# Kernel tuning notes

Measured on AMD Instinct MI355X. Metric: run time of the kernel, lower is better.

Reference implementation:

```python
import jax, jax.numpy as jnp
import numpy as np

NEG_SLOPE = 0.2  # PyG GATv2Conv default negative_slope


def _gatv2(h, src, dst, Wl, bl, Wr, br, att, bias, N):
    """GATv2Conv (concat=True). h: [N,Fin]; att: [H,F]; returns [N,H*F]."""
    H, F = att.shape
    xl = (h @ Wl + bl).reshape(N, H, F)  # source transform
    xr = (h @ Wr + br).reshape(N, H, F)  # target transform
    # per-edge GATv2 score: a^T LeakyReLU(xl[src] + xr[dst])
    e = jax.nn.leaky_relu(xl[src] + xr[dst], negative_slope=NEG_SLOPE)  # [E,H,F]
    logits = jnp.einsum('ehf,hf->eh', e, att)  # [E,H]
    # segment softmax over destination nodes (self-loops guarantee nonempty segments)
    m = jax.ops.segment_max(logits, dst, num_segments=N)  # [N,H]
    p = jnp.exp(logits - m[dst])
    s = jax.ops.segment_sum(p, dst, num_segments=N)  # [N,H]
    alpha = p / s[dst]  # [E,H]
    out = jax.ops.segment_sum(alpha[:, :, None] * xl[src], dst, num_segments=N)  # [N,H,F]
    return out.reshape(N, H * F) + bias


def setup_inputs() -> dict:
    key = jax.random.key(0)
    ks = jax.random.split(key, 16)
    N, E = 30000, 480000
    L, D, H, F = 50, 100, 3, 100
    W = D * H  # 300
    sc = 0.1  # keep activations stable through 5 layers
    return {
        'x': jax.random.randint(ks[0], (N,), 0, L),
        'edge_index': jax.random.randint(ks[1], (2, E), 0, N),
        'emb': jax.random.normal(ks[2], (L, D), jnp.float32),
        'Wl0': jax.random.normal(ks[3], (D, W), jnp.float32) * sc,
        'bl0': jnp.zeros((W,), jnp.float32),
        'Wr0': jax.random.normal(ks[4], (D, W), jnp.float32) * sc,
        'br0': jnp.zeros((W,), jnp.float32),
        'att0': jax.random.normal(ks[5], (H, F), jnp.float32) * sc,
        'bias0': jnp.zeros((W,), jnp.float32),
        'Wl': jax.random.normal(ks[6], (4, W, W), jnp.float32) * sc,
        'bl': jnp.zeros((4, W), jnp.float32),
        'Wr': jax.random.normal(ks[7], (4, W, W), jnp.float32) * sc,
        'br': jnp.zeros((4, W), jnp.float32),
        'att': jax.random.normal(ks[8], (4, H, F), jnp.float32) * sc,
        'bias': jnp.zeros((4, W), jnp.float32),
    }


def reference(x, edge_index, emb, Wl0, bl0, Wr0, br0, att0, bias0,
              Wl, bl, Wr, br, att, bias):
    N = x.shape[0]
    loops = jnp.arange(N)
    src = jnp.concatenate([edge_index[0], loops])  # PyG add_self_loops=True
    dst = jnp.concatenate([edge_index[1], loops])
    h = emb[x]  # node_embedding(x).squeeze()
    h = jax.nn.relu(_gatv2(h, src, dst, Wl0, bl0, Wr0, br0, att0, bias0, N))
    for i in range(4):  # remaining num_gnn_layers-1 convs, each followed by ReLU
        h = jax.nn.relu(_gatv2(h, src, dst, Wl[i], bl[i], Wr[i], br[i], att[i], bias[i], N))
    return h  # [N, heads*hidden] = [N, 300]
```

## Files before the change

kernel.cpp:

```cpp
#include <hip/hip_runtime.h>

#define NODES   30000
#define E0N     480000
#define ETOT    510000
#define D0      100
#define WDIM    300
#define NW      600
#define NEG     0.2f

typedef __bf16 bf16x8 __attribute__((ext_vector_type(8)));
typedef float  f32x4  __attribute__((ext_vector_type(4)));

__global__ void count_edges(const int* __restrict__ ei, int* __restrict__ counts) {
    int e = blockIdx.x * 256 + threadIdx.x;
    if (e >= ETOT) return;
    int d = (e < E0N) ? ei[E0N + e] : (e - E0N);
    atomicAdd(&counts[d], 1);
}

__global__ __launch_bounds__(1024) void scan_kernel(const int* __restrict__ counts,
                                                    int* __restrict__ offsets, int n) {
    __shared__ int lds[1024];
    const int CH = 32;
    int t = threadIdx.x;
    int base = t * CH;
    int loc[CH];
    int sum = 0;
    #pragma unroll
    for (int i = 0; i < CH; i++) {
        int v = (base + i < n) ? counts[base + i] : 0;
        loc[i] = sum;
        sum += v;
    }
    lds[t] = sum;
    __syncthreads();
    for (int off = 1; off < 1024; off <<= 1) {
        int v = (t >= off) ? lds[t - off] : 0;
        __syncthreads();
        lds[t] += v;
        __syncthreads();
    }
    int ex = (t == 0) ? 0 : lds[t - 1];
    #pragma unroll
    for (int i = 0; i < CH; i++) {
        int idx = base + i;
        if (idx < n) offsets[idx] = ex + loc[i];
    }
    if (t == 0) offsets[n] = lds[1023];
}

__global__ void scatter_edges(const int* __restrict__ ei, const int* __restrict__ offsets,
                              int* __restrict__ cursor, int* __restrict__ csr_src) {
    int e = blockIdx.x * 256 + threadIdx.x;
    if (e >= ETOT) return;
    int s, d;
    if (e < E0N) { s = ei[e]; d = ei[E0N + e]; }
    else         { s = e - E0N; d = s; }
    int pos = offsets[d] + atomicAdd(&cursor[d], 1);
    csr_src[pos] = s;
}

__global__ void make_bfrag(const float* __restrict__ Bl, const float* __restrict__ Br,
                           bf16x8* __restrict__ out, int K, int ksteps) {
    int t = blockIdx.x * 256 + threadIdx.x;
    int total = ksteps * 40 * 64;
    if (t >= total) return;
    int lane = t & 63;
    int n16  = (t >> 6) % 40;
    int s    = t / (64 * 40);
    int c = n16 * 16 + (lane & 15);
    union { bf16x8 v; __bf16 e[8]; } hi, lo;
    #pragma unroll
    for (int j = 0; j < 8; j++) {
        int k = s * 32 + ((lane >> 4) * 8) + j;
        float x = 0.f;
        if (k < K && c < NW)
            x = (c < WDIM) ? Bl[(size_t)k * WDIM + c] : Br[(size_t)k * WDIM + c - WDIM];
        __bf16 h = (__bf16)x;
        hi.e[j] = h;
        lo.e[j] = (__bf16)(x - (float)h);
    }
    size_t base = ((size_t)(s * 40 + n16) * 2) * 64 + lane;
    out[base]      = hi.v;
    out[base + 64] = lo.v;
}

__global__ __launch_bounds__(256) void gemm_mfma(
    const float* __restrict__ A, const int* __restrict__ xmap, int use_map,
    const bf16x8* __restrict__ Bfrag,
    const float* __restrict__ bl, const float* __restrict__ br,
    float* __restrict__ Cl, float* __restrict__ Cr,
    int M, int K, int ksteps) {

    __shared__ bf16x8 Alds[8][2][64];
    __shared__ bf16x8 Blds[8][2][64];

    int id = blockIdx.x;
    int mb = (id & 7) + 8 * (id / 40);
    int cb = (id >> 3) % 5;
    if (mb >= 235) return;

    int tid  = threadIdx.x;
    int lane = tid & 63;
    int wid  = tid >> 6;
    int wm = wid >> 1, wn = wid & 1;
    int row0 = mb * 128;

    f32x4 acc[4][4] = {};

    for (int s = 0; s < ksteps; s++) {
        int kt = s * 32;
        #pragma unroll
        for (int u0 = 0; u0 < 2; u0++) {
            int u = u0 * 256 + tid;
            int m16  = u >> 6;
            int slot = u & 63;
            int kh = slot >> 4, rl = slot & 15;
            int gr = row0 + m16 * 16 + rl;
            int gc = kt + kh * 8;
            float4 v0 = make_float4(0.f,0.f,0.f,0.f), v1 = v0;
            if (gr < M) {
                int ar = use_map ? xmap[gr] : gr;
                const float* ap = A + (size_t)ar * K + gc;
                if (gc + 4 <= K) v0 = *(const float4*)ap;
                if (gc + 8 <= K) v1 = *(const float4*)(ap + 4);
            }
            union { bf16x8 v; __bf16 e[8]; } hi, lo;
            const float* xs0 = (const float*)&v0;
            const float* xs1 = (const float*)&v1;
            #pragma unroll
            for (int j = 0; j < 8; j++) {
                float x = (j < 4) ? xs0[j] : xs1[j - 4];
                __bf16 h = (__bf16)x;
                hi.e[j] = h;
                lo.e[j] = (__bf16)(x - (float)h);
            }
            Alds[m16][0][slot] = hi.v;
            Alds[m16][1][slot] = lo.v;
        }
        {
            const float4* bsrc = (const float4*)(Bfrag + ((size_t)(s * 40 + cb * 8) * 2) * 64);
            float4* bdst = (float4*)&Blds[0][0][0];
            #pragma unroll
            for (int c = 0; c < 4; c++)
                bdst[c * 256 + tid] = bsrc[c * 256 + tid];
        }
        __syncthreads();

        bf16x8 af[4][2], bfr[4][2];
        #pragma unroll
        for (int m = 0; m < 4; m++) {
            af[m][0] = Alds[wm * 4 + m][0][lane];
            af[m][1] = Alds[wm * 4 + m][1][lane];
        }
        #pragma unroll
        for (int n = 0; n < 4; n++) {
            bfr[n][0] = Blds[wn * 4 + n][0][lane];
            bfr[n][1] = Blds[wn * 4 + n][1][lane];
        }
        #pragma unroll
        for (int m = 0; m < 4; m++)
            #pragma unroll
            for (int n = 0; n < 4; n++) {
                acc[m][n] = __builtin_amdgcn_mfma_f32_16x16x32_bf16(af[m][1], bfr[n][0], acc[m][n], 0, 0, 0);
                acc[m][n] = __builtin_amdgcn_mfma_f32_16x16x32_bf16(af[m][0], bfr[n][1], acc[m][n], 0, 0, 0);
                acc[m][n] = __builtin_amdgcn_mfma_f32_16x16x32_bf16(af[m][0], bfr[n][0], acc[m][n], 0, 0, 0);
            }
        __syncthreads();
    }

    int r0 = row0 + wm * 64;
    int c0 = cb * 128 + wn * 64;
    #pragma unroll
    for (int m = 0; m < 4; m++)
        #pragma unroll
        for (int n = 0; n < 4; n++) {
            #pragma unroll
            for (int reg = 0; reg < 4; reg++) {
                int gr = r0 + m * 16 + (lane >> 4) * 4 + reg;
                int gc = c0 + n * 16 + (lane & 15);
                if (gr < M && gc < NW) {
                    bool left = gc < WDIM;
                    int cc = left ? gc : gc - WDIM;
                    float v = acc[m][n][reg] + (left ? bl[cc] : br[cc]);
                    (left ? Cl : Cr)[(size_t)gr * WDIM + cc] = v;
                }
            }
        }
}

__global__ __launch_bounds__(256) void gat_edge_agg(
    const float* __restrict__ xl, const float* __restrict__ xr,
    const int* __restrict__ offsets, const int* __restrict__ csr_src,
    const float* __restrict__ att, const float* __restrict__ bias,
    float* __restrict__ fout) {
    __shared__ float st[4][64][8];
    int wid  = threadIdx.x >> 6;
    int lane = threadIdx.x & 63;
    int node = blockIdx.x * 2 + (wid >> 1);
    int sub  = wid & 1;
    int r = lane & 3;
    bool c0 = lane < 50;
    bool c1 = lane < 36;

    float2 aw2[3], xr2[3];
    const float2* xrrow = (const float2*)(xr + (size_t)node * WDIM);
    #pragma unroll
    for (int j = 0; j < 3; j++) {
        int i = lane + 64 * j;
        if (i < 150) {
            aw2[j].x = att[2 * i]; aw2[j].y = att[2 * i + 1];
            xr2[j] = xrrow[i];
        } else {
            aw2[j].x = 0.f; aw2[j].y = 0.f;
            xr2[j].x = 0.f; xr2[j].y = 0.f;
        }
    }

    float mq = -1e38f, sq = 0.f;
    float2 acc2[3] = {};

    int beg = offsets[node], end = offsets[node + 1];
    int half = (end - beg + 1) >> 1;
    int lo = beg + sub * half;
    int hi = sub ? end : beg + half;

    for (int i = lo; i < hi; i += 2) {
        bool act_b = (i + 1) < hi;
        int sa = csr_src[i];
        int sb = csr_src[act_b ? i + 1 : i];
        const float2* ra = (const float2*)(xl + (size_t)sa * WDIM);
        const float2* rb = (const float2*)(xl + (size_t)sb * WDIM);
        float2 va[3], vb[3];
        va[0] = ra[lane];      vb[0] = rb[lane];
        va[1] = ra[lane + 64]; vb[1] = rb[lane + 64];
        if (lane < 22) { va[2] = ra[lane + 128]; vb[2] = rb[lane + 128]; }
        else { va[2].x = va[2].y = vb[2].x = vb[2].y = 0.f; }

        float qa[3], qb[3];
        #pragma unroll
        for (int j = 0; j < 3; j++) {
            float tax = va[j].x + xr2[j].x; tax = fmaxf(tax, NEG * tax);
            float tay = va[j].y + xr2[j].y; tay = fmaxf(tay, NEG * tay);
            float tbx = vb[j].x + xr2[j].x; tbx = fmaxf(tbx, NEG * tbx);
            float tby = vb[j].y + xr2[j].y; tby = fmaxf(tby, NEG * tby);
            qa[j] = tax * aw2[j].x + tay * aw2[j].y;
            qb[j] = tbx * aw2[j].x + tby * aw2[j].y;
        }
        float pa0 = c0 ? qa[0] : 0.f;
        float pa1 = (c0 ? 0.f : qa[0]) + (c1 ? qa[1] : 0.f);
        float pa2 = (c1 ? 0.f : qa[1]) + qa[2];
        float pb0 = c0 ? qb[0] : 0.f;
        float pb1 = (c0 ? 0.f : qb[0]) + (c1 ? qb[1] : 0.f);
        float pb2 = (c1 ? 0.f : qb[1]) + qb[2];

        pa0 += __shfl_xor(pa0, 1, 64); pa1 += __shfl_xor(pa1, 1, 64); pa2 += __shfl_xor(pa2, 1, 64);
        pb0 += __shfl_xor(pb0, 1, 64); pb1 += __shfl_xor(pb1, 1, 64); pb2 += __shfl_xor(pb2, 1, 64);
        pa0 += __shfl_xor(pa0, 2, 64); pa1 += __shfl_xor(pa1, 2, 64); pa2 += __shfl_xor(pa2, 2, 64);
        pb0 += __shfl_xor(pb0, 2, 64); pb1 += __shfl_xor(pb1, 2, 64); pb2 += __shfl_xor(pb2, 2, 64);
        float sqa = (r == 1) ? pa1 : ((r == 2) ? pa2 : pa0);
        float sqb = (r == 1) ? pb1 : ((r == 2) ? pb2 : pb0);
        sqa += __shfl_xor(sqa, 4, 64);  sqb += __shfl_xor(sqb, 4, 64);
        sqa += __shfl_xor(sqa, 8, 64);  sqb += __shfl_xor(sqb, 8, 64);
        sqa += __shfl_xor(sqa, 16, 64); sqb += __shfl_xor(sqb, 16, 64);
        sqa += __shfl_xor(sqa, 32, 64); sqb += __shfl_xor(sqb, 32, 64);
        if (!act_b) sqb = -3e38f;

        float hiq = fmaxf(sqa, sqb);
        if (__any(hiq > mq + 8.f)) {
            float nmq = fmaxf(mq, hiq);
            float eq = __expf(mq - nmq);
            sq *= eq;
            float e0 = __shfl(eq, 0, 64), e1 = __shfl(eq, 1, 64), e2 = __shfl(eq, 2, 64);
            float ej0 = c0 ? e0 : e1, ej1 = c1 ? e1 : e2;
            acc2[0].x *= ej0; acc2[0].y *= ej0;
            acc2[1].x *= ej1; acc2[1].y *= ej1;
            acc2[2].x *= e2;  acc2[2].y *= e2;
            mq = nmq;
        }
        float cqa = __expf(sqa - mq), cqb = __expf(sqb - mq);
        sq += cqa + cqb;
        float ca0 = __shfl(cqa, 0, 64), ca1 = __shfl(cqa, 1, 64), ca2 = __shfl(cqa, 2, 64);
        float cb0 = __shfl(cqb, 0, 64), cb1 = __shfl(cqb, 1, 64), cb2 = __shfl(cqb, 2, 64);
        float caj[3] = { c0 ? ca0 : ca1, c1 ? ca1 : ca2, ca2 };
        float cbj[3] = { c0 ? cb0 : cb1, c1 ? cb1 : cb2, cb2 };
        #pragma unroll
        for (int j = 0; j < 3; j++) {
            acc2[j].x = fmaf(caj[j], va[j].x, acc2[j].x);
            acc2[j].y = fmaf(caj[j], va[j].y, acc2[j].y);
            acc2[j].x = fmaf(cbj[j], vb[j].x, acc2[j].x);
            acc2[j].y = fmaf(cbj[j], vb[j].y, acc2[j].y);
        }
    }

    st[wid][lane][0] = mq;
    st[wid][lane][1] = sq;
    st[wid][lane][2] = acc2[0].x; st[wid][lane][3] = acc2[0].y;
    st[wid][lane][4] = acc2[1].x; st[wid][lane][5] = acc2[1].y;
    st[wid][lane][6] = acc2[2].x; st[wid][lane][7] = acc2[2].y;
    __syncthreads();
    if (sub) return;

    float m1 = st[wid ^ 1][lane][0];
    float s1 = st[wid ^ 1][lane][1];
    float2 o1[3];
    o1[0].x = st[wid ^ 1][lane][2]; o1[0].y = st[wid ^ 1][lane][3];
    o1[1].x = st[wid ^ 1][lane][4]; o1[1].y = st[wid ^ 1][lane][5];
    o1[2].x = st[wid ^ 1][lane][6]; o1[2].y = st[wid ^ 1][lane][7];

    float M  = fmaxf(mq, m1);
    float ea = __expf(mq - M), eb = __expf(m1 - M);
    float sF = sq * ea + s1 * eb;
    float iq = 1.f / sF;
    float ea0 = __shfl(ea, 0, 64), ea1 = __shfl(ea, 1, 64), ea2 = __shfl(ea, 2, 64);
    float eb0 = __shfl(eb, 0, 64), eb1 = __shfl(eb, 1, 64), eb2 = __shfl(eb, 2, 64);
    float i0  = __shfl(iq, 0, 64), i1  = __shfl(iq, 1, 64), i2  = __shfl(iq, 2, 64);
    float eaj[3]  = { c0 ? ea0 : ea1, c1 ? ea1 : ea2, ea2 };
    float ebj[3]  = { c0 ? eb0 : eb1, c1 ? eb1 : eb2, eb2 };
    float isel[3] = { c0 ? i0 : i1,  c1 ? i1 : i2,  i2 };

    #pragma unroll
    for (int j = 0; j < 3; j++) {
        int fi = lane + 64 * j;
        if (fi < 150) {
            float ax = acc2[j].x * eaj[j] + o1[j].x * ebj[j];
            float ay = acc2[j].y * eaj[j] + o1[j].y * ebj[j];
            float2 o;
            o.x = fmaxf(ax * isel[j] + bias[2 * fi],     0.f);
            o.y = fmaxf(ay * isel[j] + bias[2 * fi + 1], 0.f);
            *(float2*)(fout + (size_t)node * WDIM + 2 * fi) = o;
        }
    }
}

static inline size_t align256(size_t x) { return (x + 255) & ~(size_t)255; }

extern "C" void kernel_launch(void* const* d_in, const int* in_sizes, int n_in,
                              void* d_out, int out_size, void* d_ws, size_t ws_size,
                              hipStream_t stream) {
    const int*   x     = (const int*)d_in[0];
    const int*   ei    = (const int*)d_in[1];
    const float* emb   = (const float*)d_in[2];
    const float* Wl0   = (const float*)d_in[3];
    const float* bl0   = (const float*)d_in[4];
    const float* Wr0   = (const float*)d_in[5];
    const float* br0   = (const float*)d_in[6];
    const float* att0  = (const float*)d_in[7];
    const float* bias0 = (const float*)d_in[8];
    const float* Wl    = (const float*)d_in[9];
    const float* bl    = (const float*)d_in[10];
    const float* Wr    = (const float*)d_in[11];
    const float* br    = (const float*)d_in[12];
    const float* att   = (const float*)d_in[13];
    const float* bias  = (const float*)d_in[14];

    char* ws = (char*)d_ws;
    size_t off = 0;
    float* h      = (float*)(ws + off); off = align256(off + (size_t)NODES * WDIM * 4);
    float* xlb    = (float*)(ws + off); off = align256(off + (size_t)NODES * WDIM * 4);
    float* xrb    = (float*)(ws + off); off = align256(off + (size_t)NODES * WDIM * 4);
    int* counts   = (int*)(ws + off);   off = align256(off + (size_t)NODES * 4);
    int* cursor   = (int*)(ws + off);   off = align256(off + (size_t)NODES * 4);
    int* offsets  = (int*)(ws + off);   off = align256(off + (size_t)(NODES + 1) * 4);
    int* csr_src  = (int*)(ws + off);   off = align256(off + (size_t)ETOT * 4);
    bf16x8* bfrag[5];
    bfrag[0] = (bf16x8*)(ws + off); off = align256(off + (size_t)4 * 40 * 2 * 64 * 16);
    for (int i = 1; i < 5; i++) {
        bfrag[i] = (bf16x8*)(ws + off); off = align256(off + (size_t)10 * 40 * 2 * 64 * 16);
    }

    float* out = (float*)d_out;

    make_bfrag<<<(4 * 40 * 64 + 255) / 256, 256, 0, stream>>>(Wl0, Wr0, bfrag[0], D0, 4);
    for (int i = 0; i < 4; i++)
        make_bfrag<<<(10 * 40 * 64 + 255) / 256, 256, 0, stream>>>(
            Wl + (size_t)i * WDIM * WDIM, Wr + (size_t)i * WDIM * WDIM, bfrag[i + 1], WDIM, 10);

    hipMemsetAsync(counts, 0, (size_t)NODES * 4, stream);
    hipMemsetAsync(cursor, 0, (size_t)NODES * 4, stream);
    count_edges<<<(ETOT + 255) / 256, 256, 0, stream>>>(ei, counts);
    scan_kernel<<<1, 1024, 0, stream>>>(counts, offsets, NODES);
    scatter_edges<<<(ETOT + 255) / 256, 256, 0, stream>>>(ei, offsets, cursor, csr_src);

    int agg_blocks = NODES / 2;

    gemm_mfma<<<1200, 256, 0, stream>>>(emb, x, 1, bfrag[0], bl0, br0, xlb, xrb, NODES, D0, 4);
    gat_edge_agg<<<agg_blocks, 256, 0, stream>>>(xlb, xrb, offsets, csr_src, att0, bias0, h);

    for (int i = 0; i < 4; i++) {
        float* dst = (i == 3) ? out : h;
        gemm_mfma<<<1200, 256, 0, stream>>>(h, nullptr, 0, bfrag[i + 1], bl + i * WDIM, br + i * WDIM,
                                            xlb, xrb, NODES, WDIM, 10);
        gat_edge_agg<<<agg_blocks, 256, 0, stream>>>(xlb, xrb, offsets, csr_src,
                                                     att + (size_t)i * WDIM,
                                                     bias + (size_t)i * WDIM, dst);
    }
}
```

Measured before the change: 889.2 us.

## Store source-side features as padded bf16 to halve edge gather traffic

The GEMM epilogue now writes the source-transform output xl as bf16 into rows padded to 320 elements, and the edge aggregation kernel gathers these 16-bit values and widens them to float in registers. This roughly halves the bytes read per edge in the gather-heavy aggregation, at the cost of reduced precision in both the attention logits and the aggregated messages. The padded columns are zeroed once with a memset. The five weight-fragment preparation launches are also merged into a single kernel to cut launch count.

```diff
diff --git a/kernel.cpp b/kernel.cpp
--- a/kernel.cpp
+++ b/kernel.cpp
@@ -7,6 +7,7 @@
 #define WDIM    300
 #define NW      600
 #define NEG     0.2f
+#define XLP     320
 
 typedef __bf16 bf16x8 __attribute__((ext_vector_type(8)));
 typedef float  f32x4  __attribute__((ext_vector_type(4)));
@@ -60,11 +61,8 @@
     csr_src[pos] = s;
 }
 
-__global__ void make_bfrag(const float* __restrict__ Bl, const float* __restrict__ Br,
-                           bf16x8* __restrict__ out, int K, int ksteps) {
-    int t = blockIdx.x * 256 + threadIdx.x;
-    int total = ksteps * 40 * 64;
-    if (t >= total) return;
+__device__ __forceinline__ void bfrag_one(const float* Bl, const float* Br,
+                                          bf16x8* out, int K, int t) {
     int lane = t & 63;
     int n16  = (t >> 6) % 40;
     int s    = t / (64 * 40);
@@ -85,11 +83,28 @@
     out[base + 64] = lo.v;
 }
 
+__global__ void make_bfrag_all(const float* __restrict__ Wl0, const float* __restrict__ Wr0,
+                               const float* __restrict__ Wl, const float* __restrict__ Wr,
+                               bf16x8* __restrict__ frag0, bf16x8* __restrict__ frag1,
+                               size_t fragstride) {
+    int t = blockIdx.x * 256 + threadIdx.x;
+    const int L0 = 4 * 40 * 64, LN = 10 * 40 * 64;
+    if (t < L0) {
+        bfrag_one(Wl0, Wr0, frag0, D0, t);
+    } else {
+        int u = t - L0;
+        int layer = u / LN;
+        if (layer >= 4) return;
+        bfrag_one(Wl + (size_t)layer * WDIM * WDIM, Wr + (size_t)layer * WDIM * WDIM,
+                  frag1 + layer * fragstride, WDIM, u - layer * LN);
+    }
+}
+
 __global__ __launch_bounds__(256) void gemm_mfma(
     const float* __restrict__ A, const int* __restrict__ xmap, int use_map,
     const bf16x8* __restrict__ Bfrag,
     const float* __restrict__ bl, const float* __restrict__ br,
-    float* __restrict__ Cl, float* __restrict__ Cr,
+    ushort* __restrict__ Cl16, float* __restrict__ Cr,
     int M, int K, int ksteps) {
 
     __shared__ bf16x8 Alds[8][2][64];
@@ -180,17 +195,21 @@
                 int gr = r0 + m * 16 + (lane >> 4) * 4 + reg;
                 int gc = c0 + n * 16 + (lane & 15);
                 if (gr < M && gc < NW) {
-                    bool left = gc < WDIM;
-                    int cc = left ? gc : gc - WDIM;
-                    float v = acc[m][n][reg] + (left ? bl[cc] : br[cc]);
-                    (left ? Cl : Cr)[(size_t)gr * WDIM + cc] = v;
+                    if (gc < WDIM) {
+                        float v = acc[m][n][reg] + bl[gc];
+                        __bf16 b = (__bf16)v;
+                        Cl16[(size_t)gr * XLP + gc] = *(ushort*)&b;
+                    } else {
+                        int cc = gc - WDIM;
+                        Cr[(size_t)gr * WDIM + cc] = acc[m][n][reg] + br[cc];
+                    }
                 }
             }
         }
 }
 
 __global__ __launch_bounds__(256) void gat_edge_agg(
-    const float* __restrict__ xl, const float* __restrict__ xr,
+    const ushort* __restrict__ xl, const float* __restrict__ xr,
     const int* __restrict__ offsets, const int* __restrict__ csr_src,
     const float* __restrict__ att, const float* __restrict__ bias,
     float* __restrict__ fout) {
@@ -229,13 +248,26 @@
         bool act_b = (i + 1) < hi;
         int sa = csr_src[i];
         int sb = csr_src[act_b ? i + 1 : i];
-        const float2* ra = (const float2*)(xl + (size_t)sa * WDIM);
-        const float2* rb = (const float2*)(xl + (size_t)sb * WDIM);
+        const ushort* ra = xl + (size_t)sa * XLP;
+        const ushort* rb = xl + (size_t)sb * XLP;
+        ushort2 ua[3], ub[3];
+        ua[0] = *(const ushort2*)(ra + 2 * lane);
+        ub[0] = *(const ushort2*)(rb + 2 * lane);
+        ua[1] = *(const ushort2*)(ra + 2 * (lane + 64));
+        ub[1] = *(const ushort2*)(rb + 2 * (lane + 64));
+        if (lane < 32) {
+            ua[2] = *(const ushort2*)(ra + 2 * (lane + 128));
+            ub[2] = *(const ushort2*)(rb + 2 * (lane + 128));
+        } else { ua[2].x = ua[2].y = ub[2].x = ub[2].y = 0; }
+
         float2 va[3], vb[3];
-        va[0] = ra[lane];      vb[0] = rb[lane];
-        va[1] = ra[lane + 64]; vb[1] = rb[lane + 64];
-        if (lane < 22) { va[2] = ra[lane + 128]; vb[2] = rb[lane + 128]; }
-        else { va[2].x = va[2].y = vb[2].x = vb[2].y = 0.f; }
+        #pragma unroll
+        for (int j = 0; j < 3; j++) {
+            va[j].x = __uint_as_float(((unsigned)ua[j].x) << 16);
+            va[j].y = __uint_as_float(((unsigned)ua[j].y) << 16);
+            vb[j].x = __uint_as_float(((unsigned)ub[j].x) << 16);
+            vb[j].y = __uint_as_float(((unsigned)ub[j].y) << 16);
+        }
 
         float qa[3], qb[3];
         #pragma unroll
@@ -356,25 +388,27 @@
 
     char* ws = (char*)d_ws;
     size_t off = 0;
-    float* h      = (float*)(ws + off); off = align256(off + (size_t)NODES * WDIM * 4);
-    float* xlb    = (float*)(ws + off); off = align256(off + (size_t)NODES * WDIM * 4);
-    float* xrb    = (float*)(ws + off); off = align256(off + (size_t)NODES * WDIM * 4);
-    int* counts   = (int*)(ws + off);   off = align256(off + (size_t)NODES * 4);
-    int* cursor   = (int*)(ws + off);   off = align256(off + (size_t)NODES * 4);
-    int* offsets  = (int*)(ws + off);   off = align256(off + (size_t)(NODES + 1) * 4);
-    int* csr_src  = (int*)(ws + off);   off = align256(off + (size_t)ETOT * 4);
-    bf16x8* bfrag[5];
-    bfrag[0] = (bf16x8*)(ws + off); off = align256(off + (size_t)4 * 40 * 2 * 64 * 16);
-    for (int i = 1; i < 5; i++) {
-        bfrag[i] = (bf16x8*)(ws + off); off = align256(off + (size_t)10 * 40 * 2 * 64 * 16);
-    }
+    float* h      = (float*)(ws + off);  off = align256(off + (size_t)NODES * WDIM * 4);
+    ushort* xlb16 = (ushort*)(ws + off); off = align256(off + (size_t)NODES * XLP * 2);
+    float* xrb    = (float*)(ws + off);  off = align256(off + (size_t)NODES * WDIM * 4);
+    int* counts   = (int*)(ws + off);    off = align256(off + (size_t)NODES * 4);
+    int* cursor   = (int*)(ws + off);    off = align256(off + (size_t)NODES * 4);
+    int* offsets  = (int*)(ws + off);    off = align256(off + (size_t)(NODES + 1) * 4);
+    int* csr_src  = (int*)(ws + off);    off = align256(off + (size_t)ETOT * 4);
+    size_t frag_l0_elems = (size_t)4 * 40 * 2 * 64;
+    size_t frag_ln_elems = (size_t)10 * 40 * 2 * 64;
+    bf16x8* bfrag0 = (bf16x8*)(ws + off); off = align256(off + frag_l0_elems * 16);
+    bf16x8* bfrag1 = (bf16x8*)(ws + off); off = align256(off + 4 * frag_ln_elems * 16);
 
     float* out = (float*)d_out;
 
-    make_bfrag<<<(4 * 40 * 64 + 255) / 256, 256, 0, stream>>>(Wl0, Wr0, bfrag[0], D0, 4);
-    for (int i = 0; i < 4; i++)
-        make_bfrag<<<(10 * 40 * 64 + 255) / 256, 256, 0, stream>>>(
-            Wl + (size_t)i * WDIM * WDIM, Wr + (size_t)i * WDIM * WDIM, bfrag[i + 1], WDIM, 10);
+    {
+        int total = 4 * 40 * 64 + 4 * 10 * 40 * 64;
+        make_bfrag_all<<<(total + 255) / 256, 256, 0, stream>>>(
+            Wl0, Wr0, Wl, Wr, bfrag0, bfrag1, frag_ln_elems);
+    }
+
+    hipMemsetAsync(xlb16, 0, (size_t)NODES * XLP * 2, stream);
 
     hipMemsetAsync(counts, 0, (size_t)NODES * 4, stream);
     hipMemsetAsync(cursor, 0, (size_t)NODES * 4, stream);
@@ -384,14 +418,15 @@
 
     int agg_blocks = NODES / 2;
 
-    gemm_mfma<<<1200, 256, 0, stream>>>(emb, x, 1, bfrag[0], bl0, br0, xlb, xrb, NODES, D0, 4);
-    gat_edge_agg<<<agg_blocks, 256, 0, stream>>>(xlb, xrb, offsets, csr_src, att0, bias0, h);
+    gemm_mfma<<<1200, 256, 0, stream>>>(emb, x, 1, bfrag0, bl0, br0, xlb16, xrb, NODES, D0, 4);
+    gat_edge_agg<<<agg_blocks, 256, 0, stream>>>(xlb16, xrb, offsets, csr_src, att0, bias0, h);
 
     for (int i = 0; i < 4; i++) {
         float* dst = (i == 3) ? out : h;
-        gemm_mfma<<<1200, 256, 0, stream>>>(h, nullptr, 0, bfrag[i + 1], bl + i * WDIM, br + i * WDIM,
-                                            xlb, xrb, NODES, WDIM, 10);
-        gat_edge_agg<<<agg_blocks, 256, 0, stream>>>(xlb, xrb, offsets, csr_src,
+        gemm_mfma<<<1200, 256, 0, stream>>>(h, nullptr, 0, bfrag1 + i * frag_ln_elems,
+                                            bl + i * WDIM, br + i * WDIM,
+                                            xlb16, xrb, NODES, WDIM, 10);
+        gat_edge_agg<<<agg_blocks, 256, 0, stream>>>(xlb16, xrb, offsets, csr_src,
                                                      att + (size_t)i * WDIM,
                                                      bias + (size_t)i * WDIM, dst);
     }
```

New measurement: 851.5 us. -4.2%, faster.
